# Optimization experiments

Measured on AMD Instinct MI355X. Metric: run time of the kernel, lower is better.

The kernel has to match this reference:

```python
import jax, jax.numpy as jnp
import numpy as np

N, T, C, H = 32, 512, 768, 1536  # batch, seq_len, dim, int(dim*expand)


def setup_inputs() -> dict:
    key = jax.random.key(0)
    ks = jax.random.split(key, 10)
    sc = lambda fan: 1.0 / np.sqrt(fan)
    return {
        "x_seq": jax.random.normal(ks[0], (N, T, C), jnp.float32),
        "sup_seq": jax.random.uniform(ks[1], (N, T, 1), jnp.float32),
        # torch nn.Linear weights are [out, in]; y = x @ W.T + b
        "W_in": jax.random.normal(ks[2], (C, C), jnp.float32) * sc(C),
        "W_out": jax.random.normal(ks[3], (C, C), jnp.float32) * sc(C),
        "W_bg": jax.random.normal(ks[4], (C, C), jnp.float32) * sc(C),
        "b_bg": jax.random.normal(ks[5], (C,), jnp.float32) * 0.01,
        "W_sg": jax.random.normal(ks[6], (C, 1), jnp.float32),
        "b_sg": jax.random.normal(ks[7], (C,), jnp.float32) * 0.01,
        "W_f1": jax.random.normal(ks[8], (H, C), jnp.float32) * sc(C),
        "b_f1": jnp.zeros((H,), jnp.float32),
        "W_f2": jax.random.normal(ks[9], (C, H), jnp.float32) * sc(H),
        "b_f2": jnp.zeros((C,), jnp.float32),
    }


def reference(x_seq, sup_seq, W_in, W_out, W_bg, b_bg, W_sg, b_sg, W_f1, b_f1, W_f2, b_f2):
    # in_proj (no bias)
    x = jnp.einsum('ntc,dc->ntd', x_seq, W_in)                      # [N,T,C]
    # per-step FFN with residual (exact erf GELU, matching torch default)
    h = jax.nn.gelu(jnp.einsum('ntc,hc->nth', x, W_f1) + b_f1, approximate=False)
    xt = x + jnp.einsum('nth,ch->ntc', h, W_f2) + b_f2              # [N,T,C]
    # input-dependent gate (base_gate * sup_to_gate)
    g = jax.nn.sigmoid(jnp.einsum('ntc,dc->ntd', xt, W_bg) + b_bg)
    g = g * jax.nn.sigmoid(jnp.einsum('nto,do->ntd', sup_seq, W_sg) + b_sg)
    # linear recurrence s_t = (1-g_t)*s_{t-1} + g_t*xt_t, s_0 = 0 -> associative scan
    a = 1.0 - g
    b = g * xt

    def combine(c1, c2):
        a1, b1 = c1
        a2, b2 = c2
        return a2 * a1, a2 * b1 + b2

    _, s = jax.lax.associative_scan(combine, (a, b), axis=1)        # [N,T,C]
    return jnp.einsum('ntc,dc->ntd', s, W_out)
```

## Files before the change

### kernel.cpp

```cpp
#include <hip/hip_runtime.h>
#include <hip/hip_bf16.h>
#include <math.h>

typedef __bf16 bf16;
typedef __attribute__((ext_vector_type(8))) __bf16 bf16x8;
typedef __attribute__((ext_vector_type(4))) __bf16 bf16x4;
typedef __attribute__((ext_vector_type(4))) float f32x4;

constexpr int BM = 128, BN = 128, BK = 32;

enum { EPI_PLAIN = 0, EPI_GELU = 1, EPI_RES = 2, EPI_GATE = 3 };

__device__ __forceinline__ void async16(const void* g, void* l) {
  __builtin_amdgcn_global_load_lds(
      (const __attribute__((address_space(1))) void*)g,
      (__attribute__((address_space(3))) void*)l, 16, 0, 0);
}

__device__ __forceinline__ void bar_lgkm() {
  asm volatile("s_waitcnt lgkmcnt(0)\n\ts_barrier" ::: "memory");
}

#define WAIT_VM(n) asm volatile("s_waitcnt vmcnt(" #n ")" ::: "memory")

template <typename CT, int EPI>
__global__ __launch_bounds__(512, 4) void gemm_bt_a(
    const bf16* __restrict__ A, const bf16* __restrict__ B, CT* __restrict__ C,
    const float* __restrict__ bias, const bf16* __restrict__ resid,
    const float* __restrict__ sup, const float* __restrict__ wsg,
    const float* __restrict__ bsg, int M, int N, int K) {
  __shared__ bf16 As[2][BM * BK];
  __shared__ bf16 Bs[2][BN * BK];

  const int tid = threadIdx.x;
  const int nwg = gridDim.x;
  const int cpx = nwg >> 3;
  const int wg = blockIdx.x;
  const int sw = (wg & 7) * cpx + (wg >> 3);
  const int ntn = N >> 7;
  const int bm = sw / ntn, bn = sw - bm * ntn;

  const int lane = tid & 63;
  const int wv = tid >> 6;
  const int wm = (wv >> 2) * 64, wn = (wv & 3) * 32;
  const int quad = lane >> 4, l16 = lane & 15;

  f32x4 acc[4][2];
#pragma unroll
  for (int i = 0; i < 4; i++)
#pragma unroll
    for (int j = 0; j < 2; j++) acc[i][j] = f32x4{0.f, 0.f, 0.f, 0.f};

  const int srow = tid >> 2;
  const int sq8 = ((tid & 3) ^ ((srow >> 1) & 3)) * 8;
  const int slot8 = (quad ^ ((l16 >> 1) & 3)) * 8;

  const bf16* pa = A + (size_t)(bm * BM + srow) * K + sq8;
  const bf16* pb = B + (size_t)(bn * BN + srow) * K + sq8;
  bf16* dA = &As[0][0] + wv * 512;
  bf16* dB = &Bs[0][0] + wv * 512;

  auto stg = [&](int buf) {
    async16(pa, dA + buf * 4096);
    async16(pb, dB + buf * 4096);
    pa += BK;
    pb += BK;
  };

  stg(0);

  const int nt = K / BK;
  for (int t = 0; t < nt; ++t) {
    const int cur = t & 1;
    if (t + 1 < nt) {
      stg(cur ^ 1);
      WAIT_VM(2);
    } else {
      WAIT_VM(0);
    }
    bar_lgkm();

    bf16x8 af[4], bfr[2];
#pragma unroll
    for (int i = 0; i < 4; i++)
      af[i] = *(const bf16x8*)&As[cur][(wm + i * 16 + l16) * BK + slot8];
#pragma unroll
    for (int j = 0; j < 2; j++)
      bfr[j] = *(const bf16x8*)&Bs[cur][(wn + j * 16 + l16) * BK + slot8];
#pragma unroll
    for (int i = 0; i < 4; i++)
#pragma unroll
      for (int j = 0; j < 2; j++)
        acc[i][j] = __builtin_amdgcn_mfma_f32_16x16x32_bf16(af[i], bfr[j], acc[i][j], 0, 0, 0);
    bar_lgkm();
  }

#pragma unroll
  for (int i = 0; i < 4; i++) {
    int row0 = bm * BM + wm + i * 16 + quad * 4;
#pragma unroll
    for (int j = 0; j < 2; j++) {
      int col = bn * BN + wn + j * 16 + l16;
#pragma unroll
      for (int r = 0; r < 4; r++) {
        int row = row0 + r;
        size_t idx = (size_t)row * N + col;
        float v = acc[i][j][r];
        if constexpr (EPI == EPI_PLAIN) {
          C[idx] = (CT)v;
        } else if constexpr (EPI == EPI_GELU) {
          v += bias[col];
          float gl = 0.5f * v * (1.0f + erff(v * 0.70710678118654752f));
          C[idx] = (CT)gl;
        } else if constexpr (EPI == EPI_RES) {
          v += bias[col] + (float)resid[idx];
          C[idx] = (CT)v;
        } else {
          v += bias[col];
          float g1 = 1.0f / (1.0f + expf(-v));
          float z = sup[row] * wsg[col] + bsg[col];
          float g2 = 1.0f / (1.0f + expf(-z));
          C[idx] = (CT)(g1 * g2);
        }
      }
    }
  }
}

constexpr int SC_CH = 32, SC_NCH = 16, SC_CW = 32;

__global__ __launch_bounds__(512) void scan2_kernel(const float* __restrict__ g,
                                                    const bf16* __restrict__ xt,
                                                    bf16* __restrict__ s, int T, int C) {
  __shared__ float lA[SC_NCH][SC_CW];
  __shared__ float lB[SC_NCH][SC_CW];
  __shared__ float lC[SC_NCH][SC_CW];
  const int cl = threadIdx.x & (SC_CW - 1);
  const int ch = threadIdx.x / SC_CW;
  const int c = blockIdx.x * SC_CW + cl;
  const int n = blockIdx.y;
  const size_t base = ((size_t)n * T + ch * SC_CH) * C + c;

  float a_arr[SC_CH], sl[SC_CH];
  float A = 1.f, B = 0.f;
#pragma unroll
  for (int t = 0; t < SC_CH; ++t) {
    size_t idx = base + (size_t)t * C;
    float gv = g[idx], xv = (float)xt[idx];
    float at = 1.0f - gv;
    a_arr[t] = at;
    B = at * B + gv * xv;
    sl[t] = B;
    A *= at;
  }
  lA[ch][cl] = A;
  lB[ch][cl] = B;
  __syncthreads();
  if (ch == 0) {
    float carry = 0.f;
#pragma unroll
    for (int j = 0; j < SC_NCH; ++j) {
      lC[j][cl] = carry;
      carry = lA[j][cl] * carry + lB[j][cl];
    }
  }
  __syncthreads();
  const float carry = lC[ch][cl];
  float P = 1.f;
#pragma unroll
  for (int t = 0; t < SC_CH; ++t) {
    P *= a_arr[t];
    s[base + (size_t)t * C] = (bf16)(sl[t] + P * carry);
  }
}

__global__ __launch_bounds__(256) void cvt5_kernel(
    const float* s0, bf16* d0, int n0, const float* s1, bf16* d1, int n1,
    const float* s2, bf16* d2, int n2, const float* s3, bf16* d3, int n3,
    const float* s4, bf16* d4, int n4) {
  const float* s; bf16* d; int n;
  switch (blockIdx.y) {
    case 0: s = s0; d = d0; n = n0; break;
    case 1: s = s1; d = d1; n = n1; break;
    case 2: s = s2; d = d2; n = n2; break;
    case 3: s = s3; d = d3; n = n3; break;
    default: s = s4; d = d4; n = n4; break;
  }
  int i = blockIdx.x * 256 + threadIdx.x;
  if (i < n) d[i] = (bf16)s[i];
}

__global__ __launch_bounds__(256) void cvtx_kernel(const float* __restrict__ in,
                                                   bf16* __restrict__ out, int n4) {
  int i = blockIdx.x * 256 + threadIdx.x;
  if (i < n4) {
    f32x4 v = *(const f32x4*)(in + (size_t)i * 4);
    bf16x4 b;
    b[0] = (bf16)v[0]; b[1] = (bf16)v[1]; b[2] = (bf16)v[2]; b[3] = (bf16)v[3];
    *(bf16x4*)(out + (size_t)i * 4) = b;
  }
}

extern "C" void kernel_launch(void* const* d_in, const int* in_sizes, int n_in,
                              void* d_out, int out_size, void* d_ws, size_t ws_size,
                              hipStream_t stream) {
  const float* x_seq = (const float*)d_in[0];
  const float* sup = (const float*)d_in[1];
  const float* W_in = (const float*)d_in[2];
  const float* W_out = (const float*)d_in[3];
  const float* W_bg = (const float*)d_in[4];
  const float* b_bg = (const float*)d_in[5];
  const float* W_sg = (const float*)d_in[6];
  const float* b_sg = (const float*)d_in[7];
  const float* W_f1 = (const float*)d_in[8];
  const float* b_f1 = (const float*)d_in[9];
  const float* W_f2 = (const float*)d_in[10];
  const float* b_f2 = (const float*)d_in[11];

  const int Nb = 32, T = 512, C = 768, H = 1536;
  const int M = Nb * T;

  char* ws = (char*)d_ws;
  size_t off = 0;
  auto alloc = [&](size_t bytes) {
    void* p = ws + off;
    off += (bytes + 255) & ~(size_t)255;
    return p;
  };
  bf16* Win_bf = (bf16*)alloc((size_t)C * C * 2);
  bf16* Wf1_bf = (bf16*)alloc((size_t)H * C * 2);
  bf16* Wf2_bf = (bf16*)alloc((size_t)C * H * 2);
  bf16* Wbg_bf = (bf16*)alloc((size_t)C * C * 2);
  bf16* Wout_bf = (bf16*)alloc((size_t)C * C * 2);
  bf16* xs_bf = (bf16*)alloc((size_t)M * C * 2);
  bf16* x_bf = (bf16*)alloc((size_t)M * C * 2);
  bf16* h_bf = (bf16*)alloc((size_t)M * H * 2);
  bf16* xt_bf = (bf16*)alloc((size_t)M * C * 2);
  float* g_f = (float*)alloc((size_t)M * C * 4);
  bf16* s_bf = x_bf;

  cvt5_kernel<<<dim3((H * C + 255) / 256, 5), 256, 0, stream>>>(
      W_in, Win_bf, C * C, W_f1, Wf1_bf, H * C, W_f2, Wf2_bf, C * H,
      W_bg, Wbg_bf, C * C, W_out, Wout_bf, C * C);
  cvtx_kernel<<<(M * C / 4 + 255) / 256, 256, 0, stream>>>(x_seq, xs_bf, M * C / 4);

  dim3 blk(512);
  gemm_bt_a<bf16, EPI_PLAIN><<<dim3((M / BM) * (C / BN)), blk, 0, stream>>>(
      xs_bf, Win_bf, x_bf, nullptr, nullptr, nullptr, nullptr, nullptr, M, C, C);
  gemm_bt_a<bf16, EPI_GELU><<<dim3((M / BM) * (H / BN)), blk, 0, stream>>>(
      x_bf, Wf1_bf, h_bf, b_f1, nullptr, nullptr, nullptr, nullptr, M, H, C);
  gemm_bt_a<bf16, EPI_RES><<<dim3((M / BM) * (C / BN)), blk, 0, stream>>>(
      h_bf, Wf2_bf, xt_bf, b_f2, x_bf, nullptr, nullptr, nullptr, M, C, H);
  gemm_bt_a<float, EPI_GATE><<<dim3((M / BM) * (C / BN)), blk, 0, stream>>>(
      xt_bf, Wbg_bf, g_f, b_bg, nullptr, sup, W_sg, b_sg, M, C, C);
  scan2_kernel<<<dim3(C / SC_CW, Nb), dim3(SC_CW * SC_NCH), 0, stream>>>(
      g_f, xt_bf, s_bf, T, C);
  gemm_bt_a<float, EPI_PLAIN><<<dim3((M / BM) * (C / BN)), blk, 0, stream>>>(
      s_bf, Wout_bf, (float*)d_out, nullptr, nullptr, nullptr, nullptr, nullptr, M, C, C);
}
```

Baseline: 378.9 us.

## Enlarge GEMM M-tile to 256 and switch to 32x32x16 MFMA

The GEMM block tile grows from 128x128 to 256x128, and each of the 8 waves now computes a 64x64 sub-tile with 32x32x16 bf16 MFMA instead of 16x16x32. The aim is better operand reuse per LDS read and fewer global loads of B per output. The cost is double the LDS per block, fewer blocks in the grid, and more accumulator registers, which may reduce occupancy under launch_bounds(512,4).

```diff
diff --git a/kernel.cpp b/kernel.cpp
--- a/kernel.cpp
+++ b/kernel.cpp
@@ -6,8 +6,9 @@
 typedef __attribute__((ext_vector_type(8))) __bf16 bf16x8;
 typedef __attribute__((ext_vector_type(4))) __bf16 bf16x4;
 typedef __attribute__((ext_vector_type(4))) float f32x4;
-
-constexpr int BM = 128, BN = 128, BK = 32;
+typedef __attribute__((ext_vector_type(16))) float f32x16;
+
+constexpr int BM = 256, BN = 128, BK = 32;
 
 enum { EPI_PLAIN = 0, EPI_GELU = 1, EPI_RES = 2, EPI_GATE = 3 };
 
@@ -42,30 +43,48 @@
 
   const int lane = tid & 63;
   const int wv = tid >> 6;
-  const int wm = (wv >> 2) * 64, wn = (wv & 3) * 32;
-  const int quad = lane >> 4, l16 = lane & 15;
-
-  f32x4 acc[4][2];
-#pragma unroll
-  for (int i = 0; i < 4; i++)
-#pragma unroll
-    for (int j = 0; j < 2; j++) acc[i][j] = f32x4{0.f, 0.f, 0.f, 0.f};
+  const int wm = (wv >> 1) * 64, wn = (wv & 1) * 64;
+  const int l32 = lane & 31, kh = lane >> 5;
+
+  f32x16 acc[2][2];
+#pragma unroll
+  for (int i = 0; i < 2; i++)
+#pragma unroll
+    for (int j = 0; j < 2; j++)
+#pragma unroll
+      for (int r = 0; r < 16; r++) acc[i][j][r] = 0.f;
 
   const int srow = tid >> 2;
   const int sq8 = ((tid & 3) ^ ((srow >> 1) & 3)) * 8;
-  const int slot8 = (quad ^ ((l16 >> 1) & 3)) * 8;
-
-  const bf16* pa = A + (size_t)(bm * BM + srow) * K + sq8;
+  const bf16* pa0 = A + (size_t)(bm * BM + srow) * K + sq8;
+  const bf16* pa1 = pa0 + (size_t)128 * K;
   const bf16* pb = B + (size_t)(bn * BN + srow) * K + sq8;
   bf16* dA = &As[0][0] + wv * 512;
   bf16* dB = &Bs[0][0] + wv * 512;
 
   auto stg = [&](int buf) {
-    async16(pa, dA + buf * 4096);
-    async16(pb, dB + buf * 4096);
-    pa += BK;
+    bf16* a = dA + buf * (BM * BK);
+    async16(pa0, a);
+    async16(pa1, a + 4096);
+    async16(pb, dB + buf * (BN * BK));
+    pa0 += BK;
+    pa1 += BK;
     pb += BK;
   };
+
+  int rA[2], swA[2], rB[2], swB[2];
+#pragma unroll
+  for (int mi = 0; mi < 2; mi++) {
+    int row = wm + mi * 32 + l32;
+    rA[mi] = row * BK;
+    swA[mi] = (row >> 1) & 3;
+  }
+#pragma unroll
+  for (int ni = 0; ni < 2; ni++) {
+    int col = wn + ni * 32 + l32;
+    rB[ni] = col * BK;
+    swB[ni] = (col >> 1) & 3;
+  }
 
   stg(0);
 
@@ -74,38 +93,45 @@
     const int cur = t & 1;
     if (t + 1 < nt) {
       stg(cur ^ 1);
-      WAIT_VM(2);
+      WAIT_VM(3);
     } else {
       WAIT_VM(0);
     }
     bar_lgkm();
 
-    bf16x8 af[4], bfr[2];
-#pragma unroll
-    for (int i = 0; i < 4; i++)
-      af[i] = *(const bf16x8*)&As[cur][(wm + i * 16 + l16) * BK + slot8];
-#pragma unroll
-    for (int j = 0; j < 2; j++)
-      bfr[j] = *(const bf16x8*)&Bs[cur][(wn + j * 16 + l16) * BK + slot8];
-#pragma unroll
-    for (int i = 0; i < 4; i++)
-#pragma unroll
-      for (int j = 0; j < 2; j++)
-        acc[i][j] = __builtin_amdgcn_mfma_f32_16x16x32_bf16(af[i], bfr[j], acc[i][j], 0, 0, 0);
+    bf16x8 a[2][2], b[2][2];
+#pragma unroll
+    for (int kk = 0; kk < 2; kk++) {
+      const int s = (kk << 1) | kh;
+#pragma unroll
+      for (int mi = 0; mi < 2; mi++)
+        a[kk][mi] = *(const bf16x8*)&As[cur][rA[mi] + ((s ^ swA[mi]) << 3)];
+#pragma unroll
+      for (int ni = 0; ni < 2; ni++)
+        b[kk][ni] = *(const bf16x8*)&Bs[cur][rB[ni] + ((s ^ swB[ni]) << 3)];
+    }
+#pragma unroll
+    for (int kk = 0; kk < 2; kk++)
+#pragma unroll
+      for (int mi = 0; mi < 2; mi++)
+#pragma unroll
+        for (int ni = 0; ni < 2; ni++)
+          acc[mi][ni] = __builtin_amdgcn_mfma_f32_32x32x16_bf16(
+              a[kk][mi], b[kk][ni], acc[mi][ni], 0, 0, 0);
     bar_lgkm();
   }
 
 #pragma unroll
-  for (int i = 0; i < 4; i++) {
-    int row0 = bm * BM + wm + i * 16 + quad * 4;
-#pragma unroll
-    for (int j = 0; j < 2; j++) {
-      int col = bn * BN + wn + j * 16 + l16;
-#pragma unroll
-      for (int r = 0; r < 4; r++) {
-        int row = row0 + r;
-        size_t idx = (size_t)row * N + col;
-        float v = acc[i][j][r];
+  for (int mi = 0; mi < 2; mi++) {
+    const int rbase = bm * BM + wm + mi * 32 + 4 * kh;
+#pragma unroll
+    for (int ni = 0; ni < 2; ni++) {
+      const int col = bn * BN + wn + ni * 32 + l32;
+#pragma unroll
+      for (int r = 0; r < 16; r++) {
+        const int row = rbase + (r & 3) + 8 * (r >> 2);
+        const size_t idx = (size_t)row * N + col;
+        float v = acc[mi][ni][r];
         if constexpr (EPI == EPI_PLAIN) {
           C[idx] = (CT)v;
         } else if constexpr (EPI == EPI_GELU) {
```

Result: slower. 396.2 us (+4.6%).

## Load B fragments directly from global into registers, dropping B LDS staging

Applied to the files above, without the earlier changes.

The GEMM no longer stages the B (weight) tile through shared memory. Each wave now loads its B fragments straight from global memory into registers, using even/odd register double-buffering across an unrolled-by-two K loop. The aim is to halve LDS traffic and footprint, which could allow more resident workgroups. In exchange, B is fetched redundantly by the two wave rows, through uncoalesced per-lane 16-byte global loads, and the waitcnt bookkeeping becomes more fragile.

```diff
diff --git a/kernel.cpp b/kernel.cpp
--- a/kernel.cpp
+++ b/kernel.cpp
@@ -30,7 +30,6 @@
     const float* __restrict__ sup, const float* __restrict__ wsg,
     const float* __restrict__ bsg, int M, int N, int K) {
   __shared__ bf16 As[2][BM * BK];
-  __shared__ bf16 Bs[2][BN * BK];
 
   const int tid = threadIdx.x;
   const int nwg = gridDim.x;
@@ -53,45 +52,61 @@
 
   const int srow = tid >> 2;
   const int sq8 = ((tid & 3) ^ ((srow >> 1) & 3)) * 8;
+  const bf16* pa = A + (size_t)(bm * BM + srow) * K + sq8;
+  bf16* dA = &As[0][0] + wv * 512;
+
+  auto stgA = [&](int buf) {
+    async16(pa, dA + buf * 4096);
+    pa += BK;
+  };
+
   const int slot8 = (quad ^ ((l16 >> 1) & 3)) * 8;
 
-  const bf16* pa = A + (size_t)(bm * BM + srow) * K + sq8;
-  const bf16* pb = B + (size_t)(bn * BN + srow) * K + sq8;
-  bf16* dA = &As[0][0] + wv * 512;
-  bf16* dB = &Bs[0][0] + wv * 512;
-
-  auto stg = [&](int buf) {
-    async16(pa, dA + buf * 4096);
-    async16(pb, dB + buf * 4096);
-    pa += BK;
-    pb += BK;
+  const bf16* pb0 = B + (size_t)(bn * BN + wn + l16) * K + quad * 8;
+  const bf16* pb1 = pb0 + (size_t)16 * K;
+
+  bf16x8 bE0, bE1, bO0, bO1;
+
+  stgA(0);
+  bE0 = *(const bf16x8*)(pb0);
+  bE1 = *(const bf16x8*)(pb1);
+
+  auto compute = [&](int cur, bf16x8 b0, bf16x8 b1) {
+    bf16x8 af[4];
+#pragma unroll
+    for (int i = 0; i < 4; i++)
+      af[i] = *(const bf16x8*)&As[cur][(wm + i * 16 + l16) * BK + slot8];
+#pragma unroll
+    for (int i = 0; i < 4; i++) {
+      acc[i][0] = __builtin_amdgcn_mfma_f32_16x16x32_bf16(af[i], b0, acc[i][0], 0, 0, 0);
+      acc[i][1] = __builtin_amdgcn_mfma_f32_16x16x32_bf16(af[i], b1, acc[i][1], 0, 0, 0);
+    }
   };
 
-  stg(0);
-
   const int nt = K / BK;
-  for (int t = 0; t < nt; ++t) {
-    const int cur = t & 1;
-    if (t + 1 < nt) {
-      stg(cur ^ 1);
-      WAIT_VM(2);
+  for (int t = 0; t < nt; t += 2) {
+    stgA(1);
+    {
+      const size_t ko = (size_t)(t + 1) * BK;
+      bO0 = *(const bf16x8*)(pb0 + ko);
+      bO1 = *(const bf16x8*)(pb1 + ko);
+    }
+    WAIT_VM(3);
+    bar_lgkm();
+    compute(0, bE0, bE1);
+    bar_lgkm();
+
+    if (t + 2 < nt) {
+      stgA(0);
+      const size_t ko = (size_t)(t + 2) * BK;
+      bE0 = *(const bf16x8*)(pb0 + ko);
+      bE1 = *(const bf16x8*)(pb1 + ko);
+      WAIT_VM(3);
     } else {
       WAIT_VM(0);
     }
     bar_lgkm();
-
-    bf16x8 af[4], bfr[2];
-#pragma unroll
-    for (int i = 0; i < 4; i++)
-      af[i] = *(const bf16x8*)&As[cur][(wm + i * 16 + l16) * BK + slot8];
-#pragma unroll
-    for (int j = 0; j < 2; j++)
-      bfr[j] = *(const bf16x8*)&Bs[cur][(wn + j * 16 + l16) * BK + slot8];
-#pragma unroll
-    for (int i = 0; i < 4; i++)
-#pragma unroll
-      for (int j = 0; j < 2; j++)
-        acc[i][j] = __builtin_amdgcn_mfma_f32_16x16x32_bf16(af[i], bfr[j], acc[i][j], 0, 0, 0);
+    compute(1, bO0, bO1);
     bar_lgkm();
   }
 
```

Result: slower. 471.4 us (+24.4%).

## Fuse fp32 input conversion into first GEMM and split loaders across 16 waves

Applied to the files above, without the earlier changes.

Removes the separate x_seq fp32-to-bf16 conversion kernel. The first GEMM now reads fp32 activations, converts them in registers and writes bf16 into LDS. All GEMMs move to 1024-thread blocks: 8 waves load A and 8 load B, each wave computes a 32x32 sub-tile, and the K loop is unrolled by two with register double-buffering for the fp32 path. This cuts an extra pass over x_seq through memory and adds more waves per tile, at the cost of halving the MFMA work per wave and raising barrier cost with more threads.

```diff
diff --git a/kernel.cpp b/kernel.cpp
--- a/kernel.cpp
+++ b/kernel.cpp
@@ -23,9 +23,10 @@
 
 #define WAIT_VM(n) asm volatile("s_waitcnt vmcnt(" #n ")" ::: "memory")
 
-template <typename CT, int EPI>
-__global__ __launch_bounds__(512, 4) void gemm_bt_a(
-    const bf16* __restrict__ A, const bf16* __restrict__ B, CT* __restrict__ C,
+template <typename CT, int EPI, int AFP32>
+__global__ __launch_bounds__(1024, 2) void gemm_bt_a(
+    const bf16* __restrict__ A, const float* __restrict__ Af,
+    const bf16* __restrict__ B, CT* __restrict__ C,
     const float* __restrict__ bias, const bf16* __restrict__ resid,
     const float* __restrict__ sup, const float* __restrict__ wsg,
     const float* __restrict__ bsg, int M, int N, int K) {
@@ -42,61 +43,100 @@
 
   const int lane = tid & 63;
   const int wv = tid >> 6;
-  const int wm = (wv >> 2) * 64, wn = (wv & 3) * 32;
+  const int wm = (wv >> 2) * 32, wn = (wv & 3) * 32;
   const int quad = lane >> 4, l16 = lane & 15;
-
-  f32x4 acc[4][2];
-#pragma unroll
-  for (int i = 0; i < 4; i++)
+  const int slot8 = (quad ^ ((l16 >> 1) & 3)) * 8;
+
+  f32x4 acc[2][2];
+#pragma unroll
+  for (int i = 0; i < 2; i++)
 #pragma unroll
     for (int j = 0; j < 2; j++) acc[i][j] = f32x4{0.f, 0.f, 0.f, 0.f};
 
-  const int srow = tid >> 2;
-  const int sq8 = ((tid & 3) ^ ((srow >> 1) & 3)) * 8;
-  const int slot8 = (quad ^ ((l16 >> 1) & 3)) * 8;
-
-  const bf16* pa = A + (size_t)(bm * BM + srow) * K + sq8;
-  const bf16* pb = B + (size_t)(bn * BN + srow) * K + sq8;
-  bf16* dA = &As[0][0] + wv * 512;
-  bf16* dB = &Bs[0][0] + wv * 512;
-
-  auto stg = [&](int buf) {
-    async16(pa, dA + buf * 4096);
-    async16(pb, dB + buf * 4096);
-    pa += BK;
-    pb += BK;
+  const bool isA = (wv < 8);
+  const int cid = tid & 511;
+  const int srow = cid >> 2;
+  const int sq8 = ((cid & 3) ^ ((srow >> 1) & 3)) * 8;
+
+  const bf16* pg = nullptr;
+  const float* pf = nullptr;
+  if (isA) {
+    if constexpr (AFP32)
+      pf = Af + (size_t)(bm * BM + srow) * K + sq8;
+    else
+      pg = A + (size_t)(bm * BM + srow) * K + sq8;
+  } else {
+    pg = B + (size_t)(bn * BN + srow) * K + sq8;
+  }
+  bf16* dst = (isA ? &As[0][0] : &Bs[0][0]) + (wv & 7) * 512;
+  bf16* wrA = &As[0][0] + cid * 8;
+
+  const int nt = K / BK;
+
+  f32x4 fE0, fE1, fO0, fO1;
+  if constexpr (AFP32) {
+    if (isA) {
+      fE0 = *(const f32x4*)pf;
+      fE1 = *(const f32x4*)(pf + 4);
+    } else {
+      async16(pg, dst);
+    }
+  } else {
+    async16(pg, dst);
+  }
+
+  auto step = [&](int buf, f32x4& c0, f32x4& c1, f32x4& n0, f32x4& n1, int t) {
+    const bool more = (t + 1) < nt;
+    if constexpr (AFP32) {
+      if (isA) {
+        if (more) {
+          const float* p = pf + (size_t)(t + 1) * BK;
+          n0 = *(const f32x4*)p;
+          n1 = *(const f32x4*)(p + 4);
+          WAIT_VM(2);
+        } else {
+          WAIT_VM(0);
+        }
+        bf16x8 v;
+        v[0] = (bf16)c0[0]; v[1] = (bf16)c0[1]; v[2] = (bf16)c0[2]; v[3] = (bf16)c0[3];
+        v[4] = (bf16)c1[0]; v[5] = (bf16)c1[1]; v[6] = (bf16)c1[2]; v[7] = (bf16)c1[3];
+        *(bf16x8*)(wrA + buf * 4096) = v;
+      } else {
+        if (more) {
+          async16(pg + (size_t)(t + 1) * BK, dst + (buf ^ 1) * 4096);
+          WAIT_VM(1);
+        } else {
+          WAIT_VM(0);
+        }
+      }
+    } else {
+      if (more) {
+        async16(pg + (size_t)(t + 1) * BK, dst + (buf ^ 1) * 4096);
+        WAIT_VM(1);
+      } else {
+        WAIT_VM(0);
+      }
+    }
+    bar_lgkm();
+
+    bf16x8 af0 = *(const bf16x8*)&As[buf][(wm + l16) * BK + slot8];
+    bf16x8 af1 = *(const bf16x8*)&As[buf][(wm + 16 + l16) * BK + slot8];
+    bf16x8 bf0 = *(const bf16x8*)&Bs[buf][(wn + l16) * BK + slot8];
+    bf16x8 bf1 = *(const bf16x8*)&Bs[buf][(wn + 16 + l16) * BK + slot8];
+    acc[0][0] = __builtin_amdgcn_mfma_f32_16x16x32_bf16(af0, bf0, acc[0][0], 0, 0, 0);
+    acc[0][1] = __builtin_amdgcn_mfma_f32_16x16x32_bf16(af0, bf1, acc[0][1], 0, 0, 0);
+    acc[1][0] = __builtin_amdgcn_mfma_f32_16x16x32_bf16(af1, bf0, acc[1][0], 0, 0, 0);
+    acc[1][1] = __builtin_amdgcn_mfma_f32_16x16x32_bf16(af1, bf1, acc[1][1], 0, 0, 0);
+    bar_lgkm();
   };
 
-  stg(0);
-
-  const int nt = K / BK;
-  for (int t = 0; t < nt; ++t) {
-    const int cur = t & 1;
-    if (t + 1 < nt) {
-      stg(cur ^ 1);
-      WAIT_VM(2);
-    } else {
-      WAIT_VM(0);
-    }
-    bar_lgkm();
-
-    bf16x8 af[4], bfr[2];
-#pragma unroll
-    for (int i = 0; i < 4; i++)
-      af[i] = *(const bf16x8*)&As[cur][(wm + i * 16 + l16) * BK + slot8];
-#pragma unroll
-    for (int j = 0; j < 2; j++)
-      bfr[j] = *(const bf16x8*)&Bs[cur][(wn + j * 16 + l16) * BK + slot8];
-#pragma unroll
-    for (int i = 0; i < 4; i++)
-#pragma unroll
-      for (int j = 0; j < 2; j++)
-        acc[i][j] = __builtin_amdgcn_mfma_f32_16x16x32_bf16(af[i], bfr[j], acc[i][j], 0, 0, 0);
-    bar_lgkm();
-  }
-
-#pragma unroll
-  for (int i = 0; i < 4; i++) {
+  for (int t = 0; t < nt; t += 2) {
+    step(0, fE0, fE1, fO0, fO1, t);
+    step(1, fO0, fO1, fE0, fE1, t + 1);
+  }
+
+#pragma unroll
+  for (int i = 0; i < 2; i++) {
     int row0 = bm * BM + wm + i * 16 + quad * 4;
 #pragma unroll
     for (int j = 0; j < 2; j++) {
@@ -190,17 +230,6 @@
   if (i < n) d[i] = (bf16)s[i];
 }
 
-__global__ __launch_bounds__(256) void cvtx_kernel(const float* __restrict__ in,
-                                                   bf16* __restrict__ out, int n4) {
-  int i = blockIdx.x * 256 + threadIdx.x;
-  if (i < n4) {
-    f32x4 v = *(const f32x4*)(in + (size_t)i * 4);
-    bf16x4 b;
-    b[0] = (bf16)v[0]; b[1] = (bf16)v[1]; b[2] = (bf16)v[2]; b[3] = (bf16)v[3];
-    *(bf16x4*)(out + (size_t)i * 4) = b;
-  }
-}
-
 extern "C" void kernel_launch(void* const* d_in, const int* in_sizes, int n_in,
                               void* d_out, int out_size, void* d_ws, size_t ws_size,
                               hipStream_t stream) {
@@ -232,7 +261,6 @@
   bf16* Wf2_bf = (bf16*)alloc((size_t)C * H * 2);
   bf16* Wbg_bf = (bf16*)alloc((size_t)C * C * 2);
   bf16* Wout_bf = (bf16*)alloc((size_t)C * C * 2);
-  bf16* xs_bf = (bf16*)alloc((size_t)M * C * 2);
   bf16* x_bf = (bf16*)alloc((size_t)M * C * 2);
   bf16* h_bf = (bf16*)alloc((size_t)M * H * 2);
   bf16* xt_bf = (bf16*)alloc((size_t)M * C * 2);
@@ -242,19 +270,18 @@
   cvt5_kernel<<<dim3((H * C + 255) / 256, 5), 256, 0, stream>>>(
       W_in, Win_bf, C * C, W_f1, Wf1_bf, H * C, W_f2, Wf2_bf, C * H,
       W_bg, Wbg_bf, C * C, W_out, Wout_bf, C * C);
-  cvtx_kernel<<<(M * C / 4 + 255) / 256, 256, 0, stream>>>(x_seq, xs_bf, M * C / 4);
-
-  dim3 blk(512);
-  gemm_bt_a<bf16, EPI_PLAIN><<<dim3((M / BM) * (C / BN)), blk, 0, stream>>>(
-      xs_bf, Win_bf, x_bf, nullptr, nullptr, nullptr, nullptr, nullptr, M, C, C);
-  gemm_bt_a<bf16, EPI_GELU><<<dim3((M / BM) * (H / BN)), blk, 0, stream>>>(
-      x_bf, Wf1_bf, h_bf, b_f1, nullptr, nullptr, nullptr, nullptr, M, H, C);
-  gemm_bt_a<bf16, EPI_RES><<<dim3((M / BM) * (C / BN)), blk, 0, stream>>>(
-      h_bf, Wf2_bf, xt_bf, b_f2, x_bf, nullptr, nullptr, nullptr, M, C, H);
-  gemm_bt_a<float, EPI_GATE><<<dim3((M / BM) * (C / BN)), blk, 0, stream>>>(
-      xt_bf, Wbg_bf, g_f, b_bg, nullptr, sup, W_sg, b_sg, M, C, C);
+
+  dim3 blk(1024);
+  gemm_bt_a<bf16, EPI_PLAIN, 1><<<dim3((M / BM) * (C / BN)), blk, 0, stream>>>(
+      nullptr, x_seq, Win_bf, x_bf, nullptr, nullptr, nullptr, nullptr, nullptr, M, C, C);
+  gemm_bt_a<bf16, EPI_GELU, 0><<<dim3((M / BM) * (H / BN)), blk, 0, stream>>>(
+      x_bf, nullptr, Wf1_bf, h_bf, b_f1, nullptr, nullptr, nullptr, nullptr, M, H, C);
+  gemm_bt_a<bf16, EPI_RES, 0><<<dim3((M / BM) * (C / BN)), blk, 0, stream>>>(
+      h_bf, nullptr, Wf2_bf, xt_bf, b_f2, x_bf, nullptr, nullptr, nullptr, M, C, H);
+  gemm_bt_a<float, EPI_GATE, 0><<<dim3((M / BM) * (C / BN)), blk, 0, stream>>>(
+      xt_bf, nullptr, Wbg_bf, g_f, b_bg, nullptr, sup, W_sg, b_sg, M, C, C);
   scan2_kernel<<<dim3(C / SC_CW, Nb), dim3(SC_CW * SC_NCH), 0, stream>>>(
       g_f, xt_bf, s_bf, T, C);
-  gemm_bt_a<float, EPI_PLAIN><<<dim3((M / BM) * (C / BN)), blk, 0, stream>>>(
-      s_bf, Wout_bf, (float*)d_out, nullptr, nullptr, nullptr, nullptr, nullptr, M, C, C);
-}
+  gemm_bt_a<float, EPI_PLAIN, 0><<<dim3((M / BM) * (C / BN)), blk, 0, stream>>>(
+      s_bf, nullptr, Wout_bf, (float*)d_out, nullptr, nullptr, nullptr, nullptr, nullptr, M, C, C);
+}
```

After: 381.4 us. No clear change (+0.6%).
